# Kernel optimization log

Measured on AMD Instinct MI355X. Metric: run time of the kernel, lower is better.

The kernel has to match this reference:

```python
import jax, jax.numpy as jnp
import numpy as np

BN_EPS = 1e-5


def setup_inputs() -> dict:
    key = jax.random.key(0)
    ks = jax.random.split(key, 4)
    B, C, N = 16, 512, 4096
    Cr = C // 4
    x = jax.random.normal(ks[0], (B, C, N), dtype=jnp.float32)
    W1 = jax.random.normal(ks[1], (Cr, C), dtype=jnp.float32) * (1.0 / np.sqrt(C))
    W2 = jax.random.normal(ks[2], (C, Cr), dtype=jnp.float32) * (1.0 / np.sqrt(Cr))
    gamma = jnp.ones((Cr,), dtype=jnp.float32)
    beta = jnp.zeros((Cr,), dtype=jnp.float32)
    running_mean = jnp.zeros((Cr,), dtype=jnp.float32)
    running_var = jnp.ones((Cr,), dtype=jnp.float32)
    return {"x": x, "W1": W1, "gamma": gamma, "beta": beta,
            "running_mean": running_mean, "running_var": running_var, "W2": W2}


def reference(x, W1, gamma, beta, running_mean, running_var, W2):
    # att[b,c] = sum_j (x x^T)[b,c,j] = sum_n x[b,c,n] * s[b,n], s = colsum over channels.
    # Algebraically identical to bmm(x, x^T).sum(-1), avoids the [B,C,C] intermediate.
    s = jnp.sum(x, axis=1)                       # [B, N]
    att = jnp.einsum('bcn,bn->bc', x, s)         # [B, C]
    # 1x1 Conv1d (no bias) on a length-1 sequence == dense matmul.
    h = jnp.einsum('oc,bc->bo', W1, att)         # [B, C/4]
    # BatchNorm1d (inference mode, running statistics)
    h = gamma * (h - running_mean) * jax.lax.rsqrt(running_var + BN_EPS) + beta
    h = jax.nn.relu(h)
    a = jax.nn.sigmoid(jnp.einsum('oc,bc->bo', W2, h))  # [B, C]
    return x * a[:, :, None]                     # [B, C, N]
```

## Files before the change

kernel.cpp:

```cpp
#include <hip/hip_runtime.h>
#include <math.h>

#define B_   16
#define C_   512
#define CR_  128
#define N_   4096
#define N4_  (N_ / 4)
#define TN   32
#define TN4  (TN / 4)
#define SUBT 2
#define NTB  (N_ / TN / SUBT)

static constexpr float BN_EPS_F = 1e-5f;

typedef float vfloat4 __attribute__((ext_vector_type(4)));

__global__ __launch_bounds__(256) void k1f_att(
        const float* __restrict__ x,
        float* __restrict__ att_part) {
    const int ntb = blockIdx.x;
    const int b   = blockIdx.y;
    const int t   = threadIdx.x;
    const int g   = t >> 3;
    const int i   = t & 7;

    __shared__ vfloat4 s_red[32][8];
    __shared__ vfloat4 s_tile4[8];

    const vfloat4* x4 = (const vfloat4*)x;
    float dacc[16];
#pragma unroll
    for (int st = 0; st < 16; ++st) dacc[st] = 0.f;

    for (int sub = 0; sub < SUBT; ++sub) {
        const int nt = ntb * SUBT + sub;
        const vfloat4* base = x4 + (size_t)b * C_ * N4_ + (size_t)nt * TN4;
        vfloat4 v[16];
        vfloat4 sacc = {0.f, 0.f, 0.f, 0.f};
#pragma unroll
        for (int st = 0; st < 16; ++st) {
            v[st] = base[(size_t)(st * 32 + g) * N4_ + i];
            sacc += v[st];
        }
        if (sub) __syncthreads();
        s_red[g][i] = sacc;
        __syncthreads();
        if (t < 8) {
            vfloat4 acc = {0.f, 0.f, 0.f, 0.f};
#pragma unroll
            for (int g2 = 0; g2 < 32; ++g2)
                acc += s_red[g2][t];
            s_tile4[t] = acc;
        }
        __syncthreads();
        const vfloat4 sv = s_tile4[i];
#pragma unroll
        for (int st = 0; st < 16; ++st)
            dacc[st] += v[st].x * sv.x + v[st].y * sv.y
                      + v[st].z * sv.z + v[st].w * sv.w;
    }

#pragma unroll
    for (int st = 0; st < 16; ++st) {
        float d = dacc[st];
        d += __shfl_xor(d, 1, 64);
        d += __shfl_xor(d, 2, 64);
        d += __shfl_xor(d, 4, 64);
        dacc[st] = d;
    }
    if (i == 0) {
        float* dst = att_part + ((size_t)ntb * B_ + b) * C_;
#pragma unroll
        for (int st = 0; st < 16; ++st)
            dst[st * 32 + g] = dacc[st];
    }
}

__global__ __launch_bounds__(256) void k2r(
        const float* __restrict__ att_part,
        float* __restrict__ att) {
    const int g = blockIdx.x * 256 + threadIdx.x;
    float acc = 0.f;
#pragma unroll 8
    for (int nb = 0; nb < NTB; ++nb)
        acc += att_part[(size_t)nb * (B_ * C_) + g];
    att[g] = acc;
}

__global__ __launch_bounds__(256) void k3a(
        const float* __restrict__ W1,
        const float* __restrict__ att,
        const float* __restrict__ gamma,
        const float* __restrict__ beta,
        const float* __restrict__ rmean,
        const float* __restrict__ rvar,
        float* __restrict__ h) {
    const int wave = threadIdx.x >> 6;
    const int lane = threadIdx.x & 63;
    const int idx  = blockIdx.x * 4 + wave;
    const int b = idx >> 7;
    const int o = idx & (CR_ - 1);
    const float* w  = W1  + (size_t)o * C_;
    const float* at = att + (size_t)b * C_;
    float acc = 0.f;
#pragma unroll
    for (int k = 0; k < C_ / 64; ++k)
        acc += w[k * 64 + lane] * at[k * 64 + lane];
#pragma unroll
    for (int off = 32; off >= 1; off >>= 1)
        acc += __shfl_down(acc, off, 64);
    if (lane == 0) {
        float v = gamma[o] * (acc - rmean[o]) * rsqrtf(rvar[o] + BN_EPS_F) + beta[o];
        h[idx] = fmaxf(v, 0.f);
    }
}

__global__ __launch_bounds__(256) void k3b(
        const float* __restrict__ W2,
        const float* __restrict__ h,
        float* __restrict__ a) {
    const int wave = threadIdx.x >> 6;
    const int lane = threadIdx.x & 63;
    const int idx  = blockIdx.x * 4 + wave;
    const int b = idx >> 9;
    const int j = idx & (C_ - 1);
    const float* w  = W2 + (size_t)j * CR_;
    const float* hp = h  + (size_t)b * CR_;
    float acc = w[lane] * hp[lane] + w[64 + lane] * hp[64 + lane];
#pragma unroll
    for (int off = 32; off >= 1; off >>= 1)
        acc += __shfl_down(acc, off, 64);
    if (lane == 0) a[idx] = 1.f / (1.f + expf(-acc));
}

__global__ __launch_bounds__(256) void k4_scale(
        const float* __restrict__ x,
        const float* __restrict__ a,
        float* __restrict__ out) {
    const int row = blockIdx.x;
    const float av = a[row];
    const vfloat4* xr = (const vfloat4*)x + (size_t)row * N4_;
    vfloat4* orow     = (vfloat4*)out     + (size_t)row * N4_;
#pragma unroll
    for (int it = 0; it < N4_ / 256; ++it) {
        const int idx = it * 256 + threadIdx.x;
        vfloat4 ov = xr[idx] * av;
        __builtin_nontemporal_store(ov, &orow[idx]);
    }
}

extern "C" void kernel_launch(void* const* d_in, const int* in_sizes, int n_in,
                              void* d_out, int out_size, void* d_ws, size_t ws_size,
                              hipStream_t stream) {
    const float* x     = (const float*)d_in[0];
    const float* W1    = (const float*)d_in[1];
    const float* gamma = (const float*)d_in[2];
    const float* beta  = (const float*)d_in[3];
    const float* rmean = (const float*)d_in[4];
    const float* rvar  = (const float*)d_in[5];
    const float* W2    = (const float*)d_in[6];
    float* out = (float*)d_out;

    float* ws       = (float*)d_ws;
    float* att_part = ws;
    float* att      = att_part + (size_t)NTB * B_ * C_;
    float* h        = att + (size_t)B_ * C_;
    float* a        = h + (size_t)B_ * CR_;

    k1f_att<<<dim3(NTB, B_), 256, 0, stream>>>(x, att_part);
    k2r<<<dim3(B_ * C_ / 256), 256, 0, stream>>>(att_part, att);
    k3a<<<dim3(B_ * CR_ / 4), 256, 0, stream>>>(W1, att, gamma, beta, rmean, rvar, h);
    k3b<<<dim3(B_ * C_ / 4), 256, 0, stream>>>(W2, h, a);
    k4_scale<<<dim3(B_ * C_), 256, 0, stream>>>(x, a, out);
}
```

Before: 75.62 us.

## Fuse partial reduction and both FC layers into one per-batch kernel

Merges the att partial-sum reduction, the W1 matvec with batchnorm and ReLU, and the W2 matvec with sigmoid into a single kernel with one 1024-thread block per batch. Intermediates stay in shared memory, which removes two kernel launches and the global round trips for att and h. The column-sum reduction in the first kernel now uses wave shuffles instead of a 32-way shared-memory loop. The cost is that the fused kernel runs only 16 blocks, so it uses very little of the GPU for the small matvec work.

```diff
diff --git a/kernel.cpp b/kernel.cpp
--- a/kernel.cpp
+++ b/kernel.cpp
@@ -21,10 +21,12 @@
     const int ntb = blockIdx.x;
     const int b   = blockIdx.y;
     const int t   = threadIdx.x;
+    const int w   = t >> 6;
+    const int l   = t & 63;
     const int g   = t >> 3;
     const int i   = t & 7;
 
-    __shared__ vfloat4 s_red[32][8];
+    __shared__ vfloat4 s_redw[4][8];
     __shared__ vfloat4 s_tile4[8];
 
     const vfloat4* x4 = (const vfloat4*)x;
@@ -42,16 +44,18 @@
             v[st] = base[(size_t)(st * 32 + g) * N4_ + i];
             sacc += v[st];
         }
+#pragma unroll
+        for (int mask = 8; mask <= 32; mask <<= 1) {
+            sacc.x += __shfl_xor(sacc.x, mask, 64);
+            sacc.y += __shfl_xor(sacc.y, mask, 64);
+            sacc.z += __shfl_xor(sacc.z, mask, 64);
+            sacc.w += __shfl_xor(sacc.w, mask, 64);
+        }
         if (sub) __syncthreads();
-        s_red[g][i] = sacc;
+        if (l < 8) s_redw[w][l] = sacc;
         __syncthreads();
-        if (t < 8) {
-            vfloat4 acc = {0.f, 0.f, 0.f, 0.f};
-#pragma unroll
-            for (int g2 = 0; g2 < 32; ++g2)
-                acc += s_red[g2][t];
-            s_tile4[t] = acc;
-        }
+        if (t < 8)
+            s_tile4[t] = s_redw[0][t] + s_redw[1][t] + s_redw[2][t] + s_redw[3][t];
         __syncthreads();
         const vfloat4 sv = s_tile4[i];
 #pragma unroll
@@ -76,61 +80,59 @@
     }
 }
 
-__global__ __launch_bounds__(256) void k2r(
+__global__ __launch_bounds__(1024) void k23(
         const float* __restrict__ att_part,
-        float* __restrict__ att) {
-    const int g = blockIdx.x * 256 + threadIdx.x;
-    float acc = 0.f;
-#pragma unroll 8
-    for (int nb = 0; nb < NTB; ++nb)
-        acc += att_part[(size_t)nb * (B_ * C_) + g];
-    att[g] = acc;
-}
-
-__global__ __launch_bounds__(256) void k3a(
         const float* __restrict__ W1,
-        const float* __restrict__ att,
         const float* __restrict__ gamma,
         const float* __restrict__ beta,
         const float* __restrict__ rmean,
         const float* __restrict__ rvar,
-        float* __restrict__ h) {
-    const int wave = threadIdx.x >> 6;
-    const int lane = threadIdx.x & 63;
-    const int idx  = blockIdx.x * 4 + wave;
-    const int b = idx >> 7;
-    const int o = idx & (CR_ - 1);
-    const float* w  = W1  + (size_t)o * C_;
-    const float* at = att + (size_t)b * C_;
-    float acc = 0.f;
+        const float* __restrict__ W2,
+        float* __restrict__ a) {
+    __shared__ float att_s[C_];
+    __shared__ float h_s[CR_];
+    const int b = blockIdx.x;
+    const int t = threadIdx.x;
+    const int w = t >> 6;
+    const int lane = t & 63;
+
+    if (t < C_) {
+        float acc = 0.f;
+#pragma unroll 8
+        for (int nb = 0; nb < NTB; ++nb)
+            acc += att_part[((size_t)nb * B_ + b) * C_ + t];
+        att_s[t] = acc;
+    }
+    __syncthreads();
+
 #pragma unroll
-    for (int k = 0; k < C_ / 64; ++k)
-        acc += w[k * 64 + lane] * at[k * 64 + lane];
+    for (int oo = 0; oo < 8; ++oo) {
+        const int o = w * 8 + oo;
+        const float* wp = W1 + (size_t)o * C_;
+        float acc = 0.f;
 #pragma unroll
-    for (int off = 32; off >= 1; off >>= 1)
-        acc += __shfl_down(acc, off, 64);
-    if (lane == 0) {
-        float v = gamma[o] * (acc - rmean[o]) * rsqrtf(rvar[o] + BN_EPS_F) + beta[o];
-        h[idx] = fmaxf(v, 0.f);
+        for (int k = 0; k < C_ / 64; ++k)
+            acc += wp[k * 64 + lane] * att_s[k * 64 + lane];
+#pragma unroll
+        for (int off = 32; off >= 1; off >>= 1)
+            acc += __shfl_down(acc, off, 64);
+        if (lane == 0) {
+            float v = gamma[o] * (acc - rmean[o]) * rsqrtf(rvar[o] + BN_EPS_F) + beta[o];
+            h_s[o] = fmaxf(v, 0.f);
+        }
     }
-}
+    __syncthreads();
 
-__global__ __launch_bounds__(256) void k3b(
-        const float* __restrict__ W2,
-        const float* __restrict__ h,
-        float* __restrict__ a) {
-    const int wave = threadIdx.x >> 6;
-    const int lane = threadIdx.x & 63;
-    const int idx  = blockIdx.x * 4 + wave;
-    const int b = idx >> 9;
-    const int j = idx & (C_ - 1);
-    const float* w  = W2 + (size_t)j * CR_;
-    const float* hp = h  + (size_t)b * CR_;
-    float acc = w[lane] * hp[lane] + w[64 + lane] * hp[64 + lane];
 #pragma unroll
-    for (int off = 32; off >= 1; off >>= 1)
-        acc += __shfl_down(acc, off, 64);
-    if (lane == 0) a[idx] = 1.f / (1.f + expf(-acc));
+    for (int jj = 0; jj < 32; ++jj) {
+        const int j = w * 32 + jj;
+        const float* wp = W2 + (size_t)j * CR_;
+        float acc = wp[lane] * h_s[lane] + wp[64 + lane] * h_s[64 + lane];
+#pragma unroll
+        for (int off = 32; off >= 1; off >>= 1)
+            acc += __shfl_down(acc, off, 64);
+        if (lane == 0) a[(size_t)b * C_ + j] = 1.f / (1.f + expf(-acc));
+    }
 }
 
 __global__ __launch_bounds__(256) void k4_scale(
@@ -163,13 +165,9 @@
 
     float* ws       = (float*)d_ws;
     float* att_part = ws;
-    float* att      = att_part + (size_t)NTB * B_ * C_;
-    float* h        = att + (size_t)B_ * C_;
-    float* a        = h + (size_t)B_ * CR_;
+    float* a        = att_part + (size_t)NTB * B_ * C_;
 
     k1f_att<<<dim3(NTB, B_), 256, 0, stream>>>(x, att_part);
-    k2r<<<dim3(B_ * C_ / 256), 256, 0, stream>>>(att_part, att);
-    k3a<<<dim3(B_ * CR_ / 4), 256, 0, stream>>>(W1, att, gamma, beta, rmean, rvar, h);
-    k3b<<<dim3(B_ * C_ / 4), 256, 0, stream>>>(W2, h, a);
+    k23<<<dim3(B_), 1024, 0, stream>>>(att_part, W1, gamma, beta, rmean, rvar, W2, a);
     k4_scale<<<dim3(B_ * C_), 256, 0, stream>>>(x, a, out);
 }
```

Result: slower. 92.63 us (+22.5%).
